# Kernel optimization log

Hardware: AMD Instinct MI355X
Metric: run time of the kernel (lower is better)

## Reference

```python
import jax, jax.numpy as jnp
import numpy as np

# Grid derived from voxel_size=[0.2,0.2,0.2], pcr=[0,-40,-3,70.4,40,1]
NX, NY, NZ, NB = 352, 400, 20, 4


def setup_inputs() -> dict:
    key = jax.random.key(0)
    N, C = 1_000_000, 64
    kp, kb, kz, ky, kx = jax.random.split(key, 5)
    points = jax.random.normal(kp, (N, C), dtype=jnp.float32)
    b = jax.random.randint(kb, (N,), 0, NB)
    z = jax.random.randint(kz, (N,), 0, NZ)
    y = jax.random.randint(ky, (N,), 0, NY)
    x = jax.random.randint(kx, (N,), 0, NX)
    coors = jnp.stack([b, z, y, x], axis=1).astype(jnp.int32)
    return {"points": points, "coors": coors}


def reference(points, coors):
    # Dynamic scatter with mean reduction (average_points=True):
    # group points sharing the same (batch, z, y, x) voxel coordinate and
    # average their features. Padded (unused) voxel slots have coor == -1
    # and zero features, so the output shape is static ([N, C]).
    N = points.shape[0]
    b, z, y, x = coors[:, 0], coors[:, 1], coors[:, 2], coors[:, 3]
    keys = ((b.astype(jnp.int64) * NZ + z) * NY + y) * NX + x  # linearized voxel id

    uniq, inv = jnp.unique(keys, return_inverse=True, size=N, fill_value=-1)
    inv = inv.reshape(-1)

    sums = jax.ops.segment_sum(points, inv, num_segments=N)          # [N, C]
    counts = jax.ops.segment_sum(jnp.ones((N,), points.dtype), inv, num_segments=N)
    voxels = sums / jnp.maximum(counts, 1.0)[:, None]

    # decode linearized keys back to (batch, z, y, x); -1 marks padding
    valid = uniq >= 0
    ux = uniq % NX
    uy = (uniq // NX) % NY
    uz = (uniq // (NX * NY)) % NZ
    ub = uniq // (NX * NY * NZ)
    voxel_coors = jnp.stack([ub, uz, uy, ux], axis=1).astype(jnp.int32)
    voxel_coors = jnp.where(valid[:, None], voxel_coors, -1)
    return voxels, voxel_coors
```

## Files before the change

### kernel.cpp

```cpp
#include <hip/hip_runtime.h>
#include <stdint.h>

#define NXc 352
#define NYc 400
#define NZc 20
#define KS  11264000
#define WORDS 176000
#define NBLKS 688
#define NCH 64

#define OFF_A     0ull
#define OFF_P     11264000ull
#define OFF_R     12672000ull
#define OFF_BP    13376000ull
#define OFF_BC    13380096ull
#define OFF_BM    13384192ull
#define OFF_NU    13388288ull
#define OFF_KEYPT 13388544ull
#define OFF_IOFF  17388544ull
#define OFF_ML    21388800ull
#define OFF_PID   23388800ull

static __device__ __forceinline__ int keyof(int4 c) {
  return ((c.x * NZc + c.y) * NYc + c.z) * NXc + c.w;
}

__global__ void k_zero(uint4* __restrict__ A4, unsigned int mA) {
  unsigned int i = blockIdx.x * 256 + threadIdx.x, s = gridDim.x * 256;
  uint4 z = make_uint4(0u, 0u, 0u, 0u);
  for (unsigned int j = i; j < mA; j += s) A4[j] = z;
}

__global__ void k_count(const int4* __restrict__ coors, unsigned int* __restrict__ A32,
                        int* __restrict__ keyPt, int n) {
  int p = blockIdx.x * 256 + threadIdx.x;
  if (p >= n) return;
  int key = keyof(coors[p]);
  keyPt[p] = key;
  atomicAdd(&A32[key >> 2], 1u << (8 * (key & 3)));
}

__global__ void k_scan1(const unsigned char* __restrict__ A, unsigned int* __restrict__ bp,
                        unsigned int* __restrict__ bc, unsigned int* __restrict__ bm) {
  int b = blockIdx.x, t = threadIdx.x;
  int w = b * 256 + t;
  unsigned int pres = 0, cnt = 0, mult = 0;
  if (w < WORDS) {
    const uint4* aw = (const uint4*)(A + (size_t)w * 64);
    unsigned long long mask = 0ull;
#pragma unroll
    for (int q = 0; q < 4; q++) {
      uint4 v = aw[q];
      unsigned int us[4] = { v.x, v.y, v.z, v.w };
#pragma unroll
      for (int i = 0; i < 4; i++) {
        unsigned int u = us[i];
#pragma unroll
        for (int bb = 0; bb < 4; bb++) {
          unsigned int byte = (u >> (8 * bb)) & 0xFFu;
          cnt += byte;
          mult += (byte >= 2u);
          if (byte) mask |= 1ull << (q * 16 + i * 4 + bb);
        }
      }
    }
    pres = (unsigned int)__popcll(mask);
  }
  __shared__ unsigned int sp[256], sc[256], sm[256];
  sp[t] = pres; sc[t] = cnt; sm[t] = mult; __syncthreads();
  for (int o = 128; o > 0; o >>= 1) {
    if (t < o) { sp[t] += sp[t + o]; sc[t] += sc[t + o]; sm[t] += sm[t + o]; }
    __syncthreads();
  }
  if (t == 0) { bp[b] = sp[0]; bc[b] = sc[0]; bm[b] = sm[0]; }
}

__global__ void k_scan2(unsigned int* __restrict__ bp, unsigned int* __restrict__ bc,
                        unsigned int* __restrict__ bm, unsigned int* __restrict__ nu,
                        unsigned int* __restrict__ ioff, int n) {
  int t = threadIdx.x;
  __shared__ unsigned int sp[256], sc[256], sm[256];
  unsigned int cp = 0, cc = 0, cm = 0;
  for (int base = 0; base < NBLKS; base += 256) {
    int i = base + t;
    unsigned int vp = (i < NBLKS) ? bp[i] : 0u;
    unsigned int vc = (i < NBLKS) ? bc[i] : 0u;
    unsigned int vm = (i < NBLKS) ? bm[i] : 0u;
    sp[t] = vp; sc[t] = vc; sm[t] = vm; __syncthreads();
    unsigned int ipv = vp, icv = vc, imv = vm;
    for (int o = 1; o < 256; o <<= 1) {
      unsigned int ap = (t >= o) ? sp[t - o] : 0u;
      unsigned int ac = (t >= o) ? sc[t - o] : 0u;
      unsigned int am = (t >= o) ? sm[t - o] : 0u;
      __syncthreads();
      ipv += ap; icv += ac; imv += am;
      sp[t] = ipv; sc[t] = icv; sm[t] = imv; __syncthreads();
    }
    if (i < NBLKS) { bp[i] = cp + ipv - vp; bc[i] = cc + icv - vc; bm[i] = cm + imv - vm; }
    unsigned int tp = sp[255], tc = sc[255], tm = sm[255];
    __syncthreads();
    cp += tp; cc += tc; cm += tm;
  }
  if (t == 0) { nu[0] = cp; nu[1] = cm; ioff[cp] = (unsigned int)n; }
}

__global__ void k_scan3(const unsigned char* __restrict__ A,
                        const unsigned int* __restrict__ bp, const unsigned int* __restrict__ bc,
                        const unsigned int* __restrict__ bm,
                        unsigned long long* __restrict__ P, unsigned int* __restrict__ R,
                        unsigned int* __restrict__ ioff, unsigned int* __restrict__ mlist,
                        float4* __restrict__ outc) {
  int b = blockIdx.x, t = threadIdx.x;
  int w = b * 256 + t;
  unsigned long long mask = 0ull;
  unsigned int uu[16];
  unsigned int pres = 0, cnt = 0, mult = 0;
  if (w < WORDS) {
    const uint4* aw = (const uint4*)(A + (size_t)w * 64);
#pragma unroll
    for (int q = 0; q < 4; q++) {
      uint4 v = aw[q];
      uu[q * 4 + 0] = v.x; uu[q * 4 + 1] = v.y; uu[q * 4 + 2] = v.z; uu[q * 4 + 3] = v.w;
    }
#pragma unroll
    for (int i = 0; i < 16; i++) {
      unsigned int u = uu[i];
#pragma unroll
      for (int bb = 0; bb < 4; bb++) {
        unsigned int byte = (u >> (8 * bb)) & 0xFFu;
        cnt += byte;
        mult += (byte >= 2u);
        if (byte) mask |= 1ull << (i * 4 + bb);
      }
    }
    pres = (unsigned int)__popcll(mask);
  }
  __shared__ unsigned int sp[256], sc[256], sm[256];
  sp[t] = pres; sc[t] = cnt; sm[t] = mult; __syncthreads();
  unsigned int ip = pres, ic = cnt, im = mult;
  for (int o = 1; o < 256; o <<= 1) {
    unsigned int ap = (t >= o) ? sp[t - o] : 0u;
    unsigned int ac = (t >= o) ? sc[t - o] : 0u;
    unsigned int am = (t >= o) ? sm[t - o] : 0u;
    __syncthreads();
    ip += ap; ic += ac; im += am;
    sp[t] = ip; sc[t] = ic; sm[t] = im; __syncthreads();
  }
  if (w < WORDS) {
    unsigned int rank  = bp[b] + ip - pres;
    unsigned int coff  = bc[b] + ic - cnt;
    unsigned int mrank = bm[b] + im - mult;
    P[w] = mask; R[w] = rank;
    for (int j = 0; j < 64; j++) {
      unsigned int byte = (uu[j >> 2] >> (8 * (j & 3))) & 0xFFu;
      if (byte) {
        ioff[rank] = coff;
        unsigned int k = (unsigned int)w * 64u + (unsigned int)j;
        unsigned int x = k % NXc; unsigned int k2 = k / NXc;
        unsigned int y = k2 % NYc; unsigned int k3 = k2 / NYc;
        unsigned int z = k3 % NZc; unsigned int bb2 = k3 / NZc;
        outc[rank] = make_float4((float)bb2, (float)z, (float)y, (float)x);
        if (byte >= 2u) mlist[mrank++] = rank;
        rank++; coff += byte;
      }
    }
  }
}

__global__ void k_scatter(const float4* __restrict__ pts, const int* __restrict__ keyPt,
                          unsigned int* __restrict__ A32,
                          const unsigned long long* __restrict__ P, const unsigned int* __restrict__ R,
                          const unsigned int* __restrict__ ioff, unsigned int* __restrict__ pid,
                          float* __restrict__ out, int n) {
  int gt = blockIdx.x * 256 + threadIdx.x;
  int p = gt >> 4, l = gt & 15;
  if (p >= n) return;
  int key = keyPt[p];
  int w = key >> 6, bit = key & 63;
  unsigned int rank = R[w] + (unsigned int)__popcll(P[w] & ((1ull << bit) - 1ull));
  unsigned int o0 = ioff[rank], o1 = ioff[rank + 1];
  if (o1 - o0 == 1u) {
    float4 v = pts[(size_t)p * 16 + l];
    ((float4*)out)[(size_t)rank * 16 + l] = v;
  } else if (l == 0) {
    unsigned int sh = 8u * (unsigned int)(key & 3);
    unsigned int old = atomicSub(&A32[key >> 2], 1u << sh);
    unsigned int intra = ((old >> sh) & 0xFFu) - 1u;
    pid[o0 + intra] = (unsigned int)p;
  }
}

__global__ void k_mg(const float4* __restrict__ pts, const unsigned int* __restrict__ pid,
                     const unsigned int* __restrict__ ioff, const unsigned int* __restrict__ mlist,
                     const unsigned int* __restrict__ nu, float* __restrict__ out) {
  unsigned int mc16 = nu[1] * 16u;
  unsigned int s = gridDim.x * 256;
  for (unsigned int gt = blockIdx.x * 256 + threadIdx.x; gt < mc16; gt += s) {
    unsigned int g = gt >> 4, l = gt & 15;
    unsigned int rank = mlist[g];
    unsigned int o0 = ioff[rank], o1 = ioff[rank + 1];
    float4 acc = make_float4(0.f, 0.f, 0.f, 0.f);
    for (unsigned int i = o0; i < o1; i++) {
      float4 v = pts[(size_t)pid[i] * 16 + l];
      acc.x += v.x; acc.y += v.y; acc.z += v.z; acc.w += v.w;
    }
    float inv = 1.0f / (float)(o1 - o0);
    acc.x *= inv; acc.y *= inv; acc.z *= inv; acc.w *= inv;
    ((float4*)out)[(size_t)rank * 16 + l] = acc;
  }
}

__global__ void k_tail(const unsigned int* __restrict__ nu, float* __restrict__ out, int n) {
  unsigned int nU = nu[0];
  unsigned int s = gridDim.x * 256;
  float4 z = make_float4(0.f, 0.f, 0.f, 0.f);
  float4 m1 = make_float4(-1.f, -1.f, -1.f, -1.f);
  for (unsigned int r = nU + blockIdx.x * 256 + threadIdx.x; r < (unsigned int)n; r += s) {
    float4* row = (float4*)out + (size_t)r * 16;
#pragma unroll
    for (int q = 0; q < 16; q++) row[q] = z;
    ((float4*)(out + (size_t)n * NCH))[r] = m1;
  }
}

extern "C" void kernel_launch(void* const* d_in, const int* in_sizes, int n_in,
                              void* d_out, int out_size, void* d_ws, size_t ws_size,
                              hipStream_t stream) {
  const float4* pts = (const float4*)d_in[0];
  const int4* coors = (const int4*)d_in[1];
  int n = in_sizes[1] / 4;
  float* out = (float*)d_out;
  char* ws = (char*)d_ws;
  unsigned char*      A    = (unsigned char*)(ws + OFF_A);
  unsigned int*       A32  = (unsigned int*)(ws + OFF_A);
  unsigned long long* P    = (unsigned long long*)(ws + OFF_P);
  unsigned int*       R    = (unsigned int*)(ws + OFF_R);
  unsigned int*       bp   = (unsigned int*)(ws + OFF_BP);
  unsigned int*       bc   = (unsigned int*)(ws + OFF_BC);
  unsigned int*       bm   = (unsigned int*)(ws + OFF_BM);
  unsigned int*       nu   = (unsigned int*)(ws + OFF_NU);
  int*                keyPt= (int*)(ws + OFF_KEYPT);
  unsigned int*       ioff = (unsigned int*)(ws + OFF_IOFF);
  unsigned int*       mlist= (unsigned int*)(ws + OFF_ML);
  unsigned int*       pid  = (unsigned int*)(ws + OFF_PID);
  float4*             outc = (float4*)(out + (size_t)n * NCH);

  k_zero   <<<2048,  256, 0, stream>>>((uint4*)A, (unsigned int)(KS / 16));
  int nb = (n + 255) / 256;
  k_count  <<<nb,    256, 0, stream>>>(coors, A32, keyPt, n);
  k_scan1  <<<NBLKS, 256, 0, stream>>>(A, bp, bc, bm);
  k_scan2  <<<1,     256, 0, stream>>>(bp, bc, bm, nu, ioff, n);
  k_scan3  <<<NBLKS, 256, 0, stream>>>(A, bp, bc, bm, P, R, ioff, mlist, outc);
  int sb = (n * 16 + 255) / 256;
  k_scatter<<<sb,    256, 0, stream>>>(pts, keyPt, A32, P, R, ioff, pid, out, n);
  k_mg     <<<2048,  256, 0, stream>>>(pts, pid, ioff, mlist, nu, out);
  k_tail   <<<2048,  256, 0, stream>>>(nu, out, n);
}
```

Measured before the change: 230.6 us.

## Add multiplicity bitmask, batch 4 points per scatter group, merge finalize kernels

Scan3 now also writes a per-word bitmask marking voxels holding two or more points. The scatter kernel can then tell singleton voxels apart from a bit test instead of loading two ioff entries. Each 16-lane group in the scatter kernel now handles 4 points, with their loads issued up front to raise memory-level parallelism. The multi-point averaging and tail-padding kernels are merged into one launch. The cost is an extra 1.4 MB mask array to write and read, plus more registers per thread in the scatter kernel.

```diff
diff --git a/kernel.cpp b/kernel.cpp
--- a/kernel.cpp
+++ b/kernel.cpp
@@ -8,18 +8,20 @@
 #define WORDS 176000
 #define NBLKS 688
 #define NCH 64
+#define RPT 4
 
 #define OFF_A     0ull
 #define OFF_P     11264000ull
 #define OFF_R     12672000ull
-#define OFF_BP    13376000ull
-#define OFF_BC    13380096ull
-#define OFF_BM    13384192ull
-#define OFF_NU    13388288ull
-#define OFF_KEYPT 13388544ull
-#define OFF_IOFF  17388544ull
-#define OFF_ML    21388800ull
-#define OFF_PID   23388800ull
+#define OFF_M     13376000ull
+#define OFF_BP    14784000ull
+#define OFF_BC    14788096ull
+#define OFF_BM    14792192ull
+#define OFF_NU    14796288ull
+#define OFF_KEYPT 14796544ull
+#define OFF_IOFF  18796544ull
+#define OFF_ML    22796800ull
+#define OFF_PID   24796800ull
 
 static __device__ __forceinline__ int keyof(int4 c) {
   return ((c.x * NZc + c.y) * NYc + c.z) * NXc + c.w;
@@ -108,11 +110,12 @@
                         const unsigned int* __restrict__ bp, const unsigned int* __restrict__ bc,
                         const unsigned int* __restrict__ bm,
                         unsigned long long* __restrict__ P, unsigned int* __restrict__ R,
+                        unsigned long long* __restrict__ M,
                         unsigned int* __restrict__ ioff, unsigned int* __restrict__ mlist,
                         float4* __restrict__ outc) {
   int b = blockIdx.x, t = threadIdx.x;
   int w = b * 256 + t;
-  unsigned long long mask = 0ull;
+  unsigned long long mask = 0ull, mmask = 0ull;
   unsigned int uu[16];
   unsigned int pres = 0, cnt = 0, mult = 0;
   if (w < WORDS) {
@@ -130,7 +133,8 @@
         unsigned int byte = (u >> (8 * bb)) & 0xFFu;
         cnt += byte;
         mult += (byte >= 2u);
-        if (byte) mask |= 1ull << (i * 4 + bb);
+        if (byte)       mask  |= 1ull << (i * 4 + bb);
+        if (byte >= 2u) mmask |= 1ull << (i * 4 + bb);
       }
     }
     pres = (unsigned int)__popcll(mask);
@@ -150,7 +154,7 @@
     unsigned int rank  = bp[b] + ip - pres;
     unsigned int coff  = bc[b] + ic - cnt;
     unsigned int mrank = bm[b] + im - mult;
-    P[w] = mask; R[w] = rank;
+    P[w] = mask; R[w] = rank; M[w] = mmask;
     for (int j = 0; j < 64; j++) {
       unsigned int byte = (uu[j >> 2] >> (8 * (j & 3))) & 0xFFu;
       if (byte) {
@@ -170,32 +174,56 @@
 __global__ void k_scatter(const float4* __restrict__ pts, const int* __restrict__ keyPt,
                           unsigned int* __restrict__ A32,
                           const unsigned long long* __restrict__ P, const unsigned int* __restrict__ R,
+                          const unsigned long long* __restrict__ M,
                           const unsigned int* __restrict__ ioff, unsigned int* __restrict__ pid,
                           float* __restrict__ out, int n) {
   int gt = blockIdx.x * 256 + threadIdx.x;
-  int p = gt >> 4, l = gt & 15;
-  if (p >= n) return;
-  int key = keyPt[p];
-  int w = key >> 6, bit = key & 63;
-  unsigned int rank = R[w] + (unsigned int)__popcll(P[w] & ((1ull << bit) - 1ull));
-  unsigned int o0 = ioff[rank], o1 = ioff[rank + 1];
-  if (o1 - o0 == 1u) {
-    float4 v = pts[(size_t)p * 16 + l];
-    ((float4*)out)[(size_t)rank * 16 + l] = v;
-  } else if (l == 0) {
-    unsigned int sh = 8u * (unsigned int)(key & 3);
-    unsigned int old = atomicSub(&A32[key >> 2], 1u << sh);
-    unsigned int intra = ((old >> sh) & 0xFFu) - 1u;
-    pid[o0 + intra] = (unsigned int)p;
-  }
-}
-
-__global__ void k_mg(const float4* __restrict__ pts, const unsigned int* __restrict__ pid,
-                     const unsigned int* __restrict__ ioff, const unsigned int* __restrict__ mlist,
-                     const unsigned int* __restrict__ nu, float* __restrict__ out) {
+  int grp = gt >> 4, l = gt & 15;
+  int pb = grp * RPT;
+  if (pb >= n) return;
+  int np = min(RPT, n - pb);
+
+  float4 v[RPT];
+#pragma unroll
+  for (int j = 0; j < RPT; j++) {
+    int p = pb + ((j < np) ? j : 0);
+    v[j] = pts[(size_t)p * 16 + l];
+  }
+  int key[RPT];
+#pragma unroll
+  for (int j = 0; j < RPT; j++) key[j] = keyPt[pb + ((j < np) ? j : 0)];
+
+  unsigned long long Pw[RPT], Mw[RPT];
+  unsigned int Rw[RPT];
+#pragma unroll
+  for (int j = 0; j < RPT; j++) {
+    int w = key[j] >> 6;
+    Pw[j] = P[w]; Mw[j] = M[w]; Rw[j] = R[w];
+  }
+
+#pragma unroll
+  for (int j = 0; j < RPT; j++) {
+    if (j >= np) break;
+    int bit = key[j] & 63;
+    unsigned int rank = Rw[j] + (unsigned int)__popcll(Pw[j] & ((1ull << bit) - 1ull));
+    if (!((Mw[j] >> bit) & 1ull)) {
+      ((float4*)out)[(size_t)rank * 16 + l] = v[j];
+    } else if (l == 0) {
+      unsigned int sh = 8u * (unsigned int)(key[j] & 3);
+      unsigned int old = atomicSub(&A32[key[j] >> 2], 1u << sh);
+      unsigned int intra = ((old >> sh) & 0xFFu) - 1u;
+      pid[ioff[rank] + intra] = (unsigned int)(pb + j);
+    }
+  }
+}
+
+__global__ void k_fin(const float4* __restrict__ pts, const unsigned int* __restrict__ pid,
+                      const unsigned int* __restrict__ ioff, const unsigned int* __restrict__ mlist,
+                      const unsigned int* __restrict__ nu, float* __restrict__ out, int n) {
+  unsigned int s = gridDim.x * 256;
+  unsigned int tid = blockIdx.x * 256 + threadIdx.x;
   unsigned int mc16 = nu[1] * 16u;
-  unsigned int s = gridDim.x * 256;
-  for (unsigned int gt = blockIdx.x * 256 + threadIdx.x; gt < mc16; gt += s) {
+  for (unsigned int gt = tid; gt < mc16; gt += s) {
     unsigned int g = gt >> 4, l = gt & 15;
     unsigned int rank = mlist[g];
     unsigned int o0 = ioff[rank], o1 = ioff[rank + 1];
@@ -208,14 +236,10 @@
     acc.x *= inv; acc.y *= inv; acc.z *= inv; acc.w *= inv;
     ((float4*)out)[(size_t)rank * 16 + l] = acc;
   }
-}
-
-__global__ void k_tail(const unsigned int* __restrict__ nu, float* __restrict__ out, int n) {
   unsigned int nU = nu[0];
-  unsigned int s = gridDim.x * 256;
   float4 z = make_float4(0.f, 0.f, 0.f, 0.f);
   float4 m1 = make_float4(-1.f, -1.f, -1.f, -1.f);
-  for (unsigned int r = nU + blockIdx.x * 256 + threadIdx.x; r < (unsigned int)n; r += s) {
+  for (unsigned int r = nU + tid; r < (unsigned int)n; r += s) {
     float4* row = (float4*)out + (size_t)r * 16;
 #pragma unroll
     for (int q = 0; q < 16; q++) row[q] = z;
@@ -235,6 +259,7 @@
   unsigned int*       A32  = (unsigned int*)(ws + OFF_A);
   unsigned long long* P    = (unsigned long long*)(ws + OFF_P);
   unsigned int*       R    = (unsigned int*)(ws + OFF_R);
+  unsigned long long* M    = (unsigned long long*)(ws + OFF_M);
   unsigned int*       bp   = (unsigned int*)(ws + OFF_BP);
   unsigned int*       bc   = (unsigned int*)(ws + OFF_BC);
   unsigned int*       bm   = (unsigned int*)(ws + OFF_BM);
@@ -250,9 +275,9 @@
   k_count  <<<nb,    256, 0, stream>>>(coors, A32, keyPt, n);
   k_scan1  <<<NBLKS, 256, 0, stream>>>(A, bp, bc, bm);
   k_scan2  <<<1,     256, 0, stream>>>(bp, bc, bm, nu, ioff, n);
-  k_scan3  <<<NBLKS, 256, 0, stream>>>(A, bp, bc, bm, P, R, ioff, mlist, outc);
-  int sb = (n * 16 + 255) / 256;
-  k_scatter<<<sb,    256, 0, stream>>>(pts, keyPt, A32, P, R, ioff, pid, out, n);
-  k_mg     <<<2048,  256, 0, stream>>>(pts, pid, ioff, mlist, nu, out);
-  k_tail   <<<2048,  256, 0, stream>>>(nu, out, n);
-}
+  k_scan3  <<<NBLKS, 256, 0, stream>>>(A, bp, bc, bm, P, R, M, ioff, mlist, outc);
+  int ngrp = (n + RPT - 1) / RPT;
+  int sb = (ngrp * 16 + 255) / 256;
+  k_scatter<<<sb,    256, 0, stream>>>(pts, keyPt, A32, P, R, M, ioff, pid, out, n);
+  k_fin    <<<2048,  256, 0, stream>>>(pts, pid, ioff, mlist, nu, out, n);
+}
```

New measurement: 209.2 us. 1.1x faster.
